# Kernel tuning notes

Hardware: AMD Instinct MI355X
Metric: run time of the kernel (lower is better)

Reference implementation:

```python
import jax, jax.numpy as jnp
import numpy as np

N = 100000      # nodes
E = 1600000     # edges (avg degree 16)
H = 128         # hidden_dim
V = 64          # vector_dim
NUM_LAYERS = 3


def setup_inputs() -> dict:
    key = jax.random.key(0)
    ks = jax.random.split(key, 16)
    s = 0.05
    inp = {
        "node_feats": jax.random.normal(ks[0], (N, 1), dtype=jnp.float32),
        "edge_index": jax.random.randint(ks[1], (2, E), 0, N, dtype=jnp.int64),
        "batch": jnp.zeros((N,), dtype=jnp.int64),
        "temperature": jnp.float32(1.0),
        "t": jnp.float32(1.0),
        # SAGEConv layer 0: in=1 -> out=H. PyG: lin_l (on aggregated, with bias), lin_r (on root, no bias)
        "Wl0": jax.random.normal(ks[2], (1, H), dtype=jnp.float32) * s,
        "bl0": jnp.zeros((H,), dtype=jnp.float32),
        "Wr0": jax.random.normal(ks[3], (1, H), dtype=jnp.float32) * s,
        # SAGEConv layers 1..2: H -> H, stacked
        "Wl": jax.random.normal(ks[4], (NUM_LAYERS - 1, H, H), dtype=jnp.float32) * s,
        "bl": jnp.zeros((NUM_LAYERS - 1, H), dtype=jnp.float32),
        "Wr": jax.random.normal(ks[5], (NUM_LAYERS - 1, H, H), dtype=jnp.float32) * s,
        # to_vector: H -> V
        "Wv": jax.random.normal(ks[6], (H, V), dtype=jnp.float32) * s,
        "bv": jnp.zeros((V,), dtype=jnp.float32),
        # mlp: (V+2) -> H -> 1
        "Wm1": jax.random.normal(ks[7], (V + 2, H), dtype=jnp.float32) * s,
        "bm1": jnp.zeros((H,), dtype=jnp.float32),
        "Wm2": jax.random.normal(ks[8], (H, 1), dtype=jnp.float32) * s,
        "bm2": jnp.zeros((1,), dtype=jnp.float32),
    }
    return inp


def reference(node_feats, edge_index, batch, temperature, t,
              Wl0, bl0, Wr0, Wl, bl, Wr, Wv, bv, Wm1, bm1, Wm2, bm2):
    n = node_feats.shape[0]
    src, dst = edge_index[0], edge_index[1]
    # in-degree for scatter-mean (clamp to 1 for isolated nodes, like PyG mean aggr)
    deg = jax.ops.segment_sum(jnp.ones((src.shape[0],), node_feats.dtype), dst, num_segments=n)
    deg = jnp.maximum(deg, 1.0)[:, None]  # (N,1)

    def sage(h, Wl_, bl_, Wr_):
        # scatter-mean of source features onto destination nodes
        agg = jax.ops.segment_sum(h[src], dst, num_segments=n) / deg
        return agg @ Wl_ + bl_ + h @ Wr_

    h = node_feats.reshape(-1, 1)  # (N,1)
    h = jax.nn.relu(sage(h, Wl0, bl0, Wr0))
    for i in range(Wl.shape[0]):
        h = jax.nn.relu(sage(h, Wl[i], bl[i], Wr[i]))

    # global_mean_pool over single graph (batch all zeros)
    num_graphs = 1
    cnt = jax.ops.segment_sum(jnp.ones((n,), h.dtype), batch, num_segments=num_graphs)
    pooled = jax.ops.segment_sum(h, batch, num_segments=num_graphs) / jnp.maximum(cnt, 1.0)[:, None]  # (1,H)

    z = pooled @ Wv + bv  # (1,V)  (no ReLU in original code path)
    extras = jnp.stack([jnp.asarray(temperature, z.dtype), jnp.asarray(t, z.dtype)]).reshape(1, 2)
    feat = jnp.concatenate([z, extras], axis=1)  # (1, V+2)
    out = jax.nn.softplus(jax.nn.relu(feat @ Wm1 + bm1) @ Wm2 + bm2)  # (1,1)
    return out
```

## Files before the change

kernel.cpp:

```cpp
#include <hip/hip_runtime.h>
#include <hip/hip_bf16.h>
#include <math.h>

#define H 128
#define BKT_SHIFT 9
#define BKT_NODES 512
#define CHUNK 2048
#define GEMM_GRID 512
#define FP8_SCALE 64.0f
#define FP8_INV (1.0f / 64.0f)

typedef __attribute__((ext_vector_type(8))) short short8;
typedef __attribute__((ext_vector_type(4))) float f32x4;
typedef __attribute__((ext_vector_type(2))) float f32x2;

static __device__ __forceinline__ ushort f2b(float v) {
    union { float f; unsigned u; } x; x.f = v;
    unsigned r = x.u + 0x7fffu + ((x.u >> 16) & 1u);
    return (ushort)(r >> 16);
}
static __device__ __forceinline__ float b2f(ushort b) {
    union { unsigned u; float f; } x; x.u = ((unsigned)b) << 16;
    return x.f;
}


__global__ void bucket_hist_kernel(const int* __restrict__ dst, int e,
                                   int* __restrict__ bucketCount, int* __restrict__ blockBase) {
    __shared__ int hist[256];
    int t = threadIdx.x;
    hist[t] = 0;
    __syncthreads();
    int base = blockIdx.x * CHUNK;
    #pragma unroll
    for (int k = 0; k < CHUNK / 256; k++) {
        int i = base + k * 256 + t;
        if (i < e) atomicAdd(&hist[dst[i] >> BKT_SHIFT], 1);
    }
    __syncthreads();
    blockBase[blockIdx.x * 256 + t] = atomicAdd(&bucketCount[t], hist[t]);
}

__global__ void bucket_scan_kernel(const int* __restrict__ bucketCount, int* __restrict__ bucketBase,
                                   int* __restrict__ rs, int n, int e) {
    if (threadIdx.x == 0 && blockIdx.x == 0) {
        int acc = 0;
        for (int i = 0; i < 256; i++) { bucketBase[i] = acc; acc += bucketCount[i]; }
        bucketBase[256] = acc;
        rs[n] = e;
    }
}

__global__ void bucket_scatter_kernel(const int* __restrict__ src, const int* __restrict__ dst, int e,
                                      const int* __restrict__ bucketBase, const int* __restrict__ blockBase,
                                      int2* __restrict__ grouped) {
    __shared__ int cur[256];
    int t = threadIdx.x;
    cur[t] = bucketBase[t] + blockBase[blockIdx.x * 256 + t];
    __syncthreads();
    int base = blockIdx.x * CHUNK;
    #pragma unroll
    for (int k = 0; k < CHUNK / 256; k++) {
        int i = base + k * 256 + t;
        if (i < e) {
            int d = dst[i];
            int pos = atomicAdd(&cur[d >> BKT_SHIFT], 1);
            int2 p; p.x = d; p.y = src[i];
            grouped[pos] = p;
        }
    }
}

__global__ void bucket_csr_kernel(const int2* __restrict__ grouped, const int* __restrict__ bucketBase,
                                  int* __restrict__ rs, int* __restrict__ csr, int n) {
    __shared__ int sdeg[BKT_NODES];
    __shared__ int sexcl[BKT_NODES];
    __shared__ int wsum[4];
    int b = blockIdx.x;
    int t = threadIdx.x;
    int nodeBase = b << BKT_SHIFT;
    int ebase = bucketBase[b], eend = bucketBase[b + 1];
    sdeg[t] = 0; sdeg[t + 256] = 0;
    __syncthreads();
    for (int e = ebase + t; e < eend; e += 256)
        atomicAdd(&sdeg[grouped[e].x - nodeBase], 1);
    __syncthreads();
    int lane = t & 63, wid = t >> 6;
    int v0 = sdeg[2 * t], v1 = sdeg[2 * t + 1];
    int p = v0 + v1;
    int x = p;
    #pragma unroll
    for (int off = 1; off < 64; off <<= 1) {
        int y = __shfl_up(x, off, 64);
        if (lane >= off) x += y;
    }
    if (lane == 63) wsum[wid] = x;
    __syncthreads();
    if (t == 0) {
        int acc = 0;
        #pragma unroll
        for (int w = 0; w < 4; w++) { int tmp = wsum[w]; wsum[w] = acc; acc += tmp; }
    }
    __syncthreads();
    int basep = wsum[wid] + x - p;
    sexcl[2 * t] = basep;
    sexcl[2 * t + 1] = basep + v0;
    int nodes = min(BKT_NODES, n - nodeBase);
    for (int i = t; i < nodes; i += 256) rs[nodeBase + i] = ebase + sexcl[i];
    sdeg[t] = 0; sdeg[t + 256] = 0;
    __syncthreads();
    for (int e = ebase + t; e < eend; e += 256) {
        int2 pr = grouped[e];
        int l = pr.x - nodeBase;
        int r = atomicAdd(&sdeg[l], 1);
        csr[ebase + sexcl[l] + r] = pr.y;
    }
}


__global__ void prep_w_kernel(const float* __restrict__ Wl, const float* __restrict__ Wr,
                              ushort* __restrict__ Btg) {
    int idx = blockIdx.x * 256 + threadIdx.x;
    if (idx >= 65536) return;
    int l = idx >> 15;
    int col = (idx >> 8) & 127;
    int k = idx & 255;
    float v = (k < 128) ? Wl[l * H * H + k * H + col] : Wr[l * H * H + (k - 128) * H + col];
    Btg[idx] = f2b(v);
}


__global__ void agg0_kernel(const float* __restrict__ x, const int* __restrict__ rs,
                            const int* __restrict__ csr, float* __restrict__ agg0, int n) {
    int i = blockIdx.x * 256 + threadIdx.x;
    if (i >= n) return;
    int a = rs[i], b = rs[i + 1];
    float s = 0.f;
    for (int e = a; e < b; e++) s += x[csr[e]];
    agg0[i] = s / (float)max(b - a, 1);
}

__global__ void expand0_kernel(const float* __restrict__ x, const float* __restrict__ agg0,
                               const float* __restrict__ Wl0, const float* __restrict__ bl0,
                               const float* __restrict__ Wr0, ushort* __restrict__ hout,
                               ushort* __restrict__ h8, int n) {
    int idx = blockIdx.x * 256 + threadIdx.x;
    if (idx >= n * 64) return;
    int i = idx >> 6, j = (idx & 63) * 2;
    float gi = agg0[i], xi = x[i];
    float v0 = fmaxf(gi * Wl0[j] + bl0[j] + xi * Wr0[j], 0.f);
    float v1 = fmaxf(gi * Wl0[j + 1] + bl0[j + 1] + xi * Wr0[j + 1], 0.f);
    ushort2 o; o.x = f2b(v0); o.y = f2b(v1);
    *(ushort2*)(hout + (size_t)i * H + j) = o;
    int p = __builtin_amdgcn_cvt_pk_fp8_f32(v0 * FP8_SCALE, v1 * FP8_SCALE, 0, false);
    h8[(size_t)i * 64 + (idx & 63)] = (ushort)p;
}


__global__ void aggregate8_kernel(const unsigned char* __restrict__ h8, const int* __restrict__ rs,
                                  const int* __restrict__ csr, ushort* __restrict__ aggb, int n) {
    int tid = threadIdx.x;
    int w = (tid >> 5) & 1;
    int node = blockIdx.x * 8 + (tid >> 6) * 2 + w;
    if (node >= n) return;
    int sl = (tid >> 3) & 3;
    int fl = tid & 7;
    int a = rs[node], b = rs[node + 1];
    f32x2 s[8];
    #pragma unroll
    for (int j = 0; j < 8; j++) s[j] = (f32x2){0.f, 0.f};

    int e = a;
    for (; e + 8 <= b; e += 8) {
        int n0 = csr[e + sl], n1 = csr[e + 4 + sl];
        uint4 u0 = *(const uint4*)(h8 + (size_t)n0 * 128 + 16 * fl);
        uint4 u1 = *(const uint4*)(h8 + (size_t)n1 * 128 + 16 * fl);
        unsigned dw[8] = {u0.x, u0.y, u0.z, u0.w, u1.x, u1.y, u1.z, u1.w};
        #pragma unroll
        for (int d = 0; d < 8; d++) {
            f32x2 lo = __builtin_amdgcn_cvt_pk_f32_fp8(dw[d], false);
            f32x2 hi = __builtin_amdgcn_cvt_pk_f32_fp8(dw[d], true);
            s[(d & 3) * 2] += lo;
            s[(d & 3) * 2 + 1] += hi;
        }
    }
    for (; e + 4 <= b; e += 4) {
        int n0 = csr[e + sl];
        uint4 u0 = *(const uint4*)(h8 + (size_t)n0 * 128 + 16 * fl);
        unsigned dw[4] = {u0.x, u0.y, u0.z, u0.w};
        #pragma unroll
        for (int d = 0; d < 4; d++) {
            f32x2 lo = __builtin_amdgcn_cvt_pk_f32_fp8(dw[d], false);
            f32x2 hi = __builtin_amdgcn_cvt_pk_f32_fp8(dw[d], true);
            s[d * 2] += lo;
            s[d * 2 + 1] += hi;
        }
    }
    if (e < b && sl < (b - e)) {
        int n0 = csr[e + sl];
        uint4 u0 = *(const uint4*)(h8 + (size_t)n0 * 128 + 16 * fl);
        unsigned dw[4] = {u0.x, u0.y, u0.z, u0.w};
        #pragma unroll
        for (int d = 0; d < 4; d++) {
            f32x2 lo = __builtin_amdgcn_cvt_pk_f32_fp8(dw[d], false);
            f32x2 hi = __builtin_amdgcn_cvt_pk_f32_fp8(dw[d], true);
            s[d * 2] += lo;
            s[d * 2 + 1] += hi;
        }
    }
    #pragma unroll
    for (int j = 0; j < 8; j++) {
        s[j].x += __shfl_xor(s[j].x, 8, 64);
        s[j].y += __shfl_xor(s[j].y, 8, 64);
        s[j].x += __shfl_xor(s[j].x, 16, 64);
        s[j].y += __shfl_xor(s[j].y, 16, 64);
    }
    if (sl == 0) {
        float inv = FP8_INV / (float)max(b - a, 1);
        short8 o0, o1;
        #pragma unroll
        for (int j = 0; j < 4; j++) {
            o0[2 * j]     = (short)f2b(s[j].x * inv);
            o0[2 * j + 1] = (short)f2b(s[j].y * inv);
            o1[2 * j]     = (short)f2b(s[j + 4].x * inv);
            o1[2 * j + 1] = (short)f2b(s[j + 4].y * inv);
        }
        ushort* dstp = aggb + (size_t)node * H + 16 * fl;
        *(short8*)dstp = o0;
        *(short8*)(dstp + 8) = o1;
    }
}


template<bool POOL>
__global__ __launch_bounds__(256, 2) void gemm_kernel(
    const ushort* __restrict__ aggb, const ushort* __restrict__ hb,
    const ushort* __restrict__ Btg,
    const float* __restrict__ bias, ushort* __restrict__ out,
    unsigned char* __restrict__ out8,
    float* __restrict__ partial, int nblk, int n) {
    __shared__ float sums[2][128];
    int tid = threadIdx.x;
    int wave = tid >> 6, lane = tid & 63;
    int l15 = lane & 15, lhi = lane >> 4;
    int colhalf = wave & 1;
    int rowsub = wave >> 1;
    int colbase = colhalf * 64;

    short8 bf[4][8];
    #pragma unroll
    for (int c2 = 0; c2 < 4; c2++) {
        const ushort* wp = Btg + (colbase + c2 * 16 + l15) * 256 + lhi * 8;
        #pragma unroll
        for (int s = 0; s < 8; s++)
            bf[c2][s] = *(const short8*)(wp + s * 32);
    }
    f32x4 bias_v[4];
    #pragma unroll
    for (int c2 = 0; c2 < 4; c2++)
        bias_v[c2] = *(const f32x4*)(bias + colbase + c2 * 16 + lhi * 4);

    f32x4 fs[4];
    #pragma unroll
    for (int c2 = 0; c2 < 4; c2++) fs[c2] = (f32x4){0.f, 0.f, 0.f, 0.f};

    for (int r0 = blockIdx.x * 32; r0 < n; r0 += nblk * 32) {
        int row = r0 + rowsub * 16 + l15;
        int arow = min(row, n - 1);
        short8 af[8];
        #pragma unroll
        for (int s = 0; s < 8; s++)
            af[s] = *(const short8*)((s < 4 ? aggb : hb) + (size_t)arow * H + (s & 3) * 32 + lhi * 8);
        f32x4 acc[4];
        #pragma unroll
        for (int c2 = 0; c2 < 4; c2++) acc[c2] = (f32x4){0.f, 0.f, 0.f, 0.f};
        #pragma unroll
        for (int s = 0; s < 8; s++) {
            #pragma unroll
            for (int c2 = 0; c2 < 4; c2++)
                acc[c2] = __builtin_amdgcn_mfma_f32_16x16x32_bf16(bf[c2][s], af[s], acc[c2], 0, 0, 0);
        }
        if (row < n) {
            if (POOL) {
                #pragma unroll
                for (int c2 = 0; c2 < 4; c2++)
                    #pragma unroll
                    for (int r = 0; r < 4; r++)
                        fs[c2][r] += fmaxf(acc[c2][r] + bias_v[c2][r], 0.f);
            } else {
                #pragma unroll
                for (int c2 = 0; c2 < 4; c2++) {
                    float v0 = fmaxf(acc[c2][0] + bias_v[c2][0], 0.f);
                    float v1 = fmaxf(acc[c2][1] + bias_v[c2][1], 0.f);
                    float v2 = fmaxf(acc[c2][2] + bias_v[c2][2], 0.f);
                    float v3 = fmaxf(acc[c2][3] + bias_v[c2][3], 0.f);
                    ushort4 o;
                    o.x = f2b(v0); o.y = f2b(v1); o.z = f2b(v2); o.w = f2b(v3);
                    *(ushort4*)(out + (size_t)row * H + colbase + c2 * 16 + lhi * 4) = o;
                    int p = __builtin_amdgcn_cvt_pk_fp8_f32(v0 * FP8_SCALE, v1 * FP8_SCALE, 0, false);
                    p = __builtin_amdgcn_cvt_pk_fp8_f32(v2 * FP8_SCALE, v3 * FP8_SCALE, p, true);
                    *(unsigned int*)(out8 + (size_t)row * 128 + colbase + c2 * 16 + lhi * 4) = (unsigned)p;
                }
            }
        }
    }

    if (POOL) {
        #pragma unroll
        for (int c2 = 0; c2 < 4; c2++) {
            #pragma unroll
            for (int m = 1; m < 16; m <<= 1) {
                #pragma unroll
                for (int r = 0; r < 4; r++)
                    fs[c2][r] += __shfl_xor(fs[c2][r], m, 64);
            }
        }
        if (l15 == 0) {
            #pragma unroll
            for (int c2 = 0; c2 < 4; c2++)
                #pragma unroll
                for (int r = 0; r < 4; r++)
                    sums[rowsub][colbase + c2 * 16 + lhi * 4 + r] = fs[c2][r];
        }
        __syncthreads();
        if (tid < 128)
            partial[tid * nblk + blockIdx.x] = sums[0][tid] + sums[1][tid];
    }
}


__global__ void pool_reduce_kernel(const float* __restrict__ partial, float* __restrict__ pooled,
                                   int nb, float invn) {
    int j = blockIdx.x;
    int t = threadIdx.x;
    float s = 0.f;
    for (int b = t; b < nb; b += 64) s += partial[j * nb + b];
    #pragma unroll
    for (int off = 32; off > 0; off >>= 1) s += __shfl_down(s, off, 64);
    if (t == 0) pooled[j] = s * invn;
}


__global__ void mlp_kernel(const float* __restrict__ pooled,
                           const float* __restrict__ Wv, const float* __restrict__ bv,
                           const float* __restrict__ temp, const float* __restrict__ tt,
                           const float* __restrict__ Wm1, const float* __restrict__ bm1,
                           const float* __restrict__ Wm2, const float* __restrict__ bm2,
                           float* __restrict__ out) {
    __shared__ float feat[66];
    __shared__ float red[2];
    int j = threadIdx.x;
    if (j < 64) {
        float s = bv[j];
        for (int k = 0; k < H; k++) s += pooled[k] * Wv[k * 64 + j];
        feat[j] = s;
    }
    if (j == 64) feat[64] = temp[0];
    if (j == 65) feat[65] = tt[0];
    __syncthreads();
    float m = bm1[j];
    for (int k = 0; k < 66; k++) m += feat[k] * Wm1[k * H + j];
    m = fmaxf(m, 0.f);
    float p = m * Wm2[j];
    #pragma unroll
    for (int off = 32; off > 0; off >>= 1) p += __shfl_down(p, off, 64);
    if ((j & 63) == 0) red[j >> 6] = p;
    __syncthreads();
    if (j == 0) {
        float x = red[0] + red[1] + bm2[0];
        out[0] = (x > 20.f) ? x : log1pf(expf(x));
    }
}


extern "C" void kernel_launch(void* const* d_in, const int* in_sizes, int n_in,
                              void* d_out, int out_size, void* d_ws, size_t ws_size,
                              hipStream_t stream) {
    const float* node_feats = (const float*)d_in[0];
    const int* edge_index = (const int*)d_in[1];
    const float* temp = (const float*)d_in[3];
    const float* tt   = (const float*)d_in[4];
    const float* Wl0 = (const float*)d_in[5];
    const float* bl0 = (const float*)d_in[6];
    const float* Wr0 = (const float*)d_in[7];
    const float* Wl  = (const float*)d_in[8];
    const float* bl  = (const float*)d_in[9];
    const float* Wr  = (const float*)d_in[10];
    const float* Wv  = (const float*)d_in[11];
    const float* bv  = (const float*)d_in[12];
    const float* Wm1 = (const float*)d_in[13];
    const float* bm1 = (const float*)d_in[14];
    const float* Wm2 = (const float*)d_in[15];
    const float* bm2 = (const float*)d_in[16];

    const int N = in_sizes[0];
    const int E = in_sizes[1] / 2;
    const int* src = edge_index;
    const int* dst = edge_index + E;

    size_t NH = (size_t)N * H;
    ushort* hA   = (ushort*)d_ws;
    ushort* hB   = hA + NH;
    ushort* aggb = hB + NH;
    ushort* Btg  = aggb + NH;
    float* agg0  = (float*)(Btg + 65536);
    int2* grouped = (int2*)(agg0 + N);
    int* csr     = (int*)(grouped + E);
    int* rs      = csr + E;
    int* bucketCount = rs + (N + 1);
    int* bucketBase  = bucketCount + 256;
    int* blockBase   = bucketBase + 257;
    int NBLK = (E + CHUNK - 1) / CHUNK;
    float* partial = (float*)(blockBase + NBLK * 256);
    float* pooled  = partial + (size_t)H * GEMM_GRID;
    unsigned char* hB8 = (unsigned char*)(pooled + H);
    unsigned char* hA8 = (unsigned char*)grouped;

    int NB = (N + BKT_NODES - 1) / BKT_NODES;

    hipMemsetAsync(bucketCount, 0, 256 * sizeof(int), stream);
    bucket_hist_kernel<<<NBLK, 256, 0, stream>>>(dst, E, bucketCount, blockBase);
    bucket_scan_kernel<<<1, 64, 0, stream>>>(bucketCount, bucketBase, rs, N, E);
    bucket_scatter_kernel<<<NBLK, 256, 0, stream>>>(src, dst, E, bucketBase, blockBase, grouped);
    bucket_csr_kernel<<<NB, 256, 0, stream>>>(grouped, bucketBase, rs, csr, N);

    prep_w_kernel<<<256, 256, 0, stream>>>(Wl, Wr, Btg);

    agg0_kernel<<<(N + 255) / 256, 256, 0, stream>>>(node_feats, rs, csr, agg0, N);
    expand0_kernel<<<((size_t)N * 64 + 255) / 256, 256, 0, stream>>>(
        node_feats, agg0, Wl0, bl0, Wr0, hA, (ushort*)hA8, N);

    aggregate8_kernel<<<(N + 7) / 8, 256, 0, stream>>>(hA8, rs, csr, aggb, N);
    gemm_kernel<false><<<GEMM_GRID, 256, 0, stream>>>(aggb, hA, Btg, bl, hB, hB8, nullptr, GEMM_GRID, N);

    aggregate8_kernel<<<(N + 7) / 8, 256, 0, stream>>>(hB8, rs, csr, aggb, N);
    gemm_kernel<true><<<GEMM_GRID, 256, 0, stream>>>(aggb, hB, Btg + 32768, bl + H, nullptr, nullptr, partial, GEMM_GRID, N);

    pool_reduce_kernel<<<H, 64, 0, stream>>>(partial, pooled, GEMM_GRID, 1.0f / (float)N);
    mlp_kernel<<<1, H, 0, stream>>>(pooled, Wv, bv, temp, tt, Wm1, bm1, Wm2, bm2, (float*)d_out);
}
```

Measured before the change: 259.4 us.

## Store FP8 features and aggregates in 16-byte feature-plane layout per node

Node features (fp8) and aggregated outputs are laid out as 8 planes of 16 features each, so each plane is a compact array of 16-byte rows. Aggregation now uses one thread per node per plane, and blocks are interleaved across planes so each plane's 1.6 MB working set can stay in cache during the random gathers. The GEMM and expand kernels are changed to read and write the planar layout. In exchange, each thread walks the full edge list of its node and repeats the csr index reads once per plane, and the GEMM reads of the aggregate become strided.

```diff
diff --git a/kernel.cpp b/kernel.cpp
--- a/kernel.cpp
+++ b/kernel.cpp
@@ -18,10 +18,6 @@
     union { float f; unsigned u; } x; x.f = v;
     unsigned r = x.u + 0x7fffu + ((x.u >> 16) & 1u);
     return (ushort)(r >> 16);
-}
-static __device__ __forceinline__ float b2f(ushort b) {
-    union { unsigned u; float f; } x; x.u = ((unsigned)b) << 16;
-    return x.f;
 }
 
 
@@ -143,98 +139,92 @@
 __global__ void expand0_kernel(const float* __restrict__ x, const float* __restrict__ agg0,
                                const float* __restrict__ Wl0, const float* __restrict__ bl0,
                                const float* __restrict__ Wr0, ushort* __restrict__ hout,
-                               ushort* __restrict__ h8, int n) {
+                               unsigned char* __restrict__ h8, int n) {
     int idx = blockIdx.x * 256 + threadIdx.x;
-    if (idx >= n * 64) return;
-    int i = idx >> 6, j = (idx & 63) * 2;
+    if (idx >= n * 8) return;
+    int i = idx >> 3, p = idx & 7;
     float gi = agg0[i], xi = x[i];
-    float v0 = fmaxf(gi * Wl0[j] + bl0[j] + xi * Wr0[j], 0.f);
-    float v1 = fmaxf(gi * Wl0[j + 1] + bl0[j + 1] + xi * Wr0[j + 1], 0.f);
-    ushort2 o; o.x = f2b(v0); o.y = f2b(v1);
-    *(ushort2*)(hout + (size_t)i * H + j) = o;
-    int p = __builtin_amdgcn_cvt_pk_fp8_f32(v0 * FP8_SCALE, v1 * FP8_SCALE, 0, false);
-    h8[(size_t)i * 64 + (idx & 63)] = (ushort)p;
-}
-
-
-__global__ void aggregate8_kernel(const unsigned char* __restrict__ h8, const int* __restrict__ rs,
-                                  const int* __restrict__ csr, ushort* __restrict__ aggb, int n) {
-    int tid = threadIdx.x;
-    int w = (tid >> 5) & 1;
-    int node = blockIdx.x * 8 + (tid >> 6) * 2 + w;
+    float v[16];
+    #pragma unroll
+    for (int k = 0; k < 16; k++) {
+        int f = p * 16 + k;
+        v[k] = fmaxf(gi * Wl0[f] + bl0[f] + xi * Wr0[f], 0.f);
+    }
+    short8 o0, o1;
+    #pragma unroll
+    for (int k = 0; k < 8; k++) { o0[k] = (short)f2b(v[k]); o1[k] = (short)f2b(v[k + 8]); }
+    ushort* hp = hout + (size_t)i * H + p * 16;
+    *(short8*)hp = o0;
+    *(short8*)(hp + 8) = o1;
+    uint4 u;
+    unsigned* up = (unsigned*)&u;
+    #pragma unroll
+    for (int d = 0; d < 4; d++) {
+        int pk = __builtin_amdgcn_cvt_pk_fp8_f32(v[4 * d] * FP8_SCALE, v[4 * d + 1] * FP8_SCALE, 0, false);
+        pk = __builtin_amdgcn_cvt_pk_fp8_f32(v[4 * d + 2] * FP8_SCALE, v[4 * d + 3] * FP8_SCALE, pk, true);
+        up[d] = (unsigned)pk;
+    }
+    *(uint4*)(h8 + ((size_t)p * n + i) * 16) = u;
+}
+
+
+__global__ void aggregate_p_kernel(const unsigned char* __restrict__ h8, const int* __restrict__ rs,
+                                   const int* __restrict__ csr, ushort* __restrict__ aggp, int n) {
+    int p = blockIdx.x & 7;
+    int node = (blockIdx.x >> 3) * 256 + threadIdx.x;
     if (node >= n) return;
-    int sl = (tid >> 3) & 3;
-    int fl = tid & 7;
+    const unsigned char* plane = h8 + (size_t)p * n * 16;
     int a = rs[node], b = rs[node + 1];
     f32x2 s[8];
     #pragma unroll
     for (int j = 0; j < 8; j++) s[j] = (f32x2){0.f, 0.f};
-
     int e = a;
-    for (; e + 8 <= b; e += 8) {
-        int n0 = csr[e + sl], n1 = csr[e + 4 + sl];
-        uint4 u0 = *(const uint4*)(h8 + (size_t)n0 * 128 + 16 * fl);
-        uint4 u1 = *(const uint4*)(h8 + (size_t)n1 * 128 + 16 * fl);
-        unsigned dw[8] = {u0.x, u0.y, u0.z, u0.w, u1.x, u1.y, u1.z, u1.w};
-        #pragma unroll
-        for (int d = 0; d < 8; d++) {
-            f32x2 lo = __builtin_amdgcn_cvt_pk_f32_fp8(dw[d], false);
-            f32x2 hi = __builtin_amdgcn_cvt_pk_f32_fp8(dw[d], true);
-            s[(d & 3) * 2] += lo;
-            s[(d & 3) * 2 + 1] += hi;
-        }
-    }
-    for (; e + 4 <= b; e += 4) {
-        int n0 = csr[e + sl];
-        uint4 u0 = *(const uint4*)(h8 + (size_t)n0 * 128 + 16 * fl);
-        unsigned dw[4] = {u0.x, u0.y, u0.z, u0.w};
+    for (; e + 2 <= b; e += 2) {
+        int n0 = csr[e], n1 = csr[e + 1];
+        uint4 u0 = *(const uint4*)(plane + (size_t)n0 * 16);
+        uint4 u1 = *(const uint4*)(plane + (size_t)n1 * 16);
+        unsigned d0[4] = {u0.x, u0.y, u0.z, u0.w};
+        unsigned d1[4] = {u1.x, u1.y, u1.z, u1.w};
         #pragma unroll
         for (int d = 0; d < 4; d++) {
-            f32x2 lo = __builtin_amdgcn_cvt_pk_f32_fp8(dw[d], false);
-            f32x2 hi = __builtin_amdgcn_cvt_pk_f32_fp8(dw[d], true);
-            s[d * 2] += lo;
-            s[d * 2 + 1] += hi;
-        }
-    }
-    if (e < b && sl < (b - e)) {
-        int n0 = csr[e + sl];
-        uint4 u0 = *(const uint4*)(h8 + (size_t)n0 * 128 + 16 * fl);
-        unsigned dw[4] = {u0.x, u0.y, u0.z, u0.w};
+            s[2 * d]     += __builtin_amdgcn_cvt_pk_f32_fp8(d0[d], false);
+            s[2 * d + 1] += __builtin_amdgcn_cvt_pk_f32_fp8(d0[d], true);
+            s[2 * d]     += __builtin_amdgcn_cvt_pk_f32_fp8(d1[d], false);
+            s[2 * d + 1] += __builtin_amdgcn_cvt_pk_f32_fp8(d1[d], true);
+        }
+    }
+    if (e < b) {
+        int n0 = csr[e];
+        uint4 u0 = *(const uint4*)(plane + (size_t)n0 * 16);
+        unsigned d0[4] = {u0.x, u0.y, u0.z, u0.w};
         #pragma unroll
         for (int d = 0; d < 4; d++) {
-            f32x2 lo = __builtin_amdgcn_cvt_pk_f32_fp8(dw[d], false);
-            f32x2 hi = __builtin_amdgcn_cvt_pk_f32_fp8(dw[d], true);
-            s[d * 2] += lo;
-            s[d * 2 + 1] += hi;
-        }
-    }
-    #pragma unroll
-    for (int j = 0; j < 8; j++) {
-        s[j].x += __shfl_xor(s[j].x, 8, 64);
-        s[j].y += __shfl_xor(s[j].y, 8, 64);
-        s[j].x += __shfl_xor(s[j].x, 16, 64);
-        s[j].y += __shfl_xor(s[j].y, 16, 64);
-    }
-    if (sl == 0) {
-        float inv = FP8_INV / (float)max(b - a, 1);
-        short8 o0, o1;
-        #pragma unroll
-        for (int j = 0; j < 4; j++) {
-            o0[2 * j]     = (short)f2b(s[j].x * inv);
-            o0[2 * j + 1] = (short)f2b(s[j].y * inv);
-            o1[2 * j]     = (short)f2b(s[j + 4].x * inv);
-            o1[2 * j + 1] = (short)f2b(s[j + 4].y * inv);
-        }
-        ushort* dstp = aggb + (size_t)node * H + 16 * fl;
-        *(short8*)dstp = o0;
-        *(short8*)(dstp + 8) = o1;
-    }
+            s[2 * d]     += __builtin_amdgcn_cvt_pk_f32_fp8(d0[d], false);
+            s[2 * d + 1] += __builtin_amdgcn_cvt_pk_f32_fp8(d0[d], true);
+        }
+    }
+    float inv = FP8_INV / (float)max(b - a, 1);
+    short8 o0, o1;
+    #pragma unroll
+    for (int d = 0; d < 2; d++) {
+        o0[4 * d]     = (short)f2b(s[2 * d].x * inv);
+        o0[4 * d + 1] = (short)f2b(s[2 * d].y * inv);
+        o0[4 * d + 2] = (short)f2b(s[2 * d + 1].x * inv);
+        o0[4 * d + 3] = (short)f2b(s[2 * d + 1].y * inv);
+        o1[4 * d]     = (short)f2b(s[2 * d + 4].x * inv);
+        o1[4 * d + 1] = (short)f2b(s[2 * d + 4].y * inv);
+        o1[4 * d + 2] = (short)f2b(s[2 * d + 5].x * inv);
+        o1[4 * d + 3] = (short)f2b(s[2 * d + 5].y * inv);
+    }
+    ushort* dstp = aggp + ((size_t)p * n + node) * 16;
+    *(short8*)dstp = o0;
+    *(short8*)(dstp + 8) = o1;
 }
 
 
 template<bool POOL>
 __global__ __launch_bounds__(256, 2) void gemm_kernel(
-    const ushort* __restrict__ aggb, const ushort* __restrict__ hb,
+    const ushort* __restrict__ aggp, const ushort* __restrict__ hb,
     const ushort* __restrict__ Btg,
     const float* __restrict__ bias, ushort* __restrict__ out,
     unsigned char* __restrict__ out8,
@@ -269,8 +259,13 @@
         int arow = min(row, n - 1);
         short8 af[8];
         #pragma unroll
-        for (int s = 0; s < 8; s++)
-            af[s] = *(const short8*)((s < 4 ? aggb : hb) + (size_t)arow * H + (s & 3) * 32 + lhi * 8);
+        for (int s = 0; s < 4; s++) {
+            int f0 = s * 32 + lhi * 8;
+            af[s] = *(const short8*)(aggp + ((size_t)(f0 >> 4) * n + arow) * 16 + (f0 & 15));
+        }
+        #pragma unroll
+        for (int s = 4; s < 8; s++)
+            af[s] = *(const short8*)(hb + (size_t)arow * H + (s & 3) * 32 + lhi * 8);
         f32x4 acc[4];
         #pragma unroll
         for (int c2 = 0; c2 < 4; c2++) acc[c2] = (f32x4){0.f, 0.f, 0.f, 0.f};
@@ -297,9 +292,10 @@
                     ushort4 o;
                     o.x = f2b(v0); o.y = f2b(v1); o.z = f2b(v2); o.w = f2b(v3);
                     *(ushort4*)(out + (size_t)row * H + colbase + c2 * 16 + lhi * 4) = o;
-                    int p = __builtin_amdgcn_cvt_pk_fp8_f32(v0 * FP8_SCALE, v1 * FP8_SCALE, 0, false);
-                    p = __builtin_amdgcn_cvt_pk_fp8_f32(v2 * FP8_SCALE, v3 * FP8_SCALE, p, true);
-                    *(unsigned int*)(out8 + (size_t)row * 128 + colbase + c2 * 16 + lhi * 4) = (unsigned)p;
+                    int pk = __builtin_amdgcn_cvt_pk_fp8_f32(v0 * FP8_SCALE, v1 * FP8_SCALE, 0, false);
+                    pk = __builtin_amdgcn_cvt_pk_fp8_f32(v2 * FP8_SCALE, v3 * FP8_SCALE, pk, true);
+                    int pl = colhalf * 4 + c2;
+                    *(unsigned*)(out8 + ((size_t)pl * n + row) * 16 + lhi * 4) = (unsigned)pk;
                 }
             }
         }
@@ -401,8 +397,8 @@
     size_t NH = (size_t)N * H;
     ushort* hA   = (ushort*)d_ws;
     ushort* hB   = hA + NH;
-    ushort* aggb = hB + NH;
-    ushort* Btg  = aggb + NH;
+    ushort* aggp = hB + NH;
+    ushort* Btg  = aggp + NH;
     float* agg0  = (float*)(Btg + 65536);
     int2* grouped = (int2*)(agg0 + N);
     int* csr     = (int*)(grouped + E);
@@ -427,14 +423,16 @@
     prep_w_kernel<<<256, 256, 0, stream>>>(Wl, Wr, Btg);
 
     agg0_kernel<<<(N + 255) / 256, 256, 0, stream>>>(node_feats, rs, csr, agg0, N);
-    expand0_kernel<<<((size_t)N * 64 + 255) / 256, 256, 0, stream>>>(
-        node_feats, agg0, Wl0, bl0, Wr0, hA, (ushort*)hA8, N);
-
-    aggregate8_kernel<<<(N + 7) / 8, 256, 0, stream>>>(hA8, rs, csr, aggb, N);
-    gemm_kernel<false><<<GEMM_GRID, 256, 0, stream>>>(aggb, hA, Btg, bl, hB, hB8, nullptr, GEMM_GRID, N);
-
-    aggregate8_kernel<<<(N + 7) / 8, 256, 0, stream>>>(hB8, rs, csr, aggb, N);
-    gemm_kernel<true><<<GEMM_GRID, 256, 0, stream>>>(aggb, hB, Btg + 32768, bl + H, nullptr, nullptr, partial, GEMM_GRID, N);
+    expand0_kernel<<<((size_t)N * 8 + 255) / 256, 256, 0, stream>>>(
+        node_feats, agg0, Wl0, bl0, Wr0, hA, hA8, N);
+
+    int AGG_GRID = ((N + 255) / 256) * 8;
+
+    aggregate_p_kernel<<<AGG_GRID, 256, 0, stream>>>(hA8, rs, csr, aggp, N);
+    gemm_kernel<false><<<GEMM_GRID, 256, 0, stream>>>(aggp, hA, Btg, bl, hB, hB8, nullptr, GEMM_GRID, N);
+
+    aggregate_p_kernel<<<AGG_GRID, 256, 0, stream>>>(hB8, rs, csr, aggp, N);
+    gemm_kernel<true><<<GEMM_GRID, 256, 0, stream>>>(aggp, hB, Btg + 32768, bl + H, nullptr, nullptr, partial, GEMM_GRID, N);
 
     pool_reduce_kernel<<<H, 64, 0, stream>>>(partial, pooled, GEMM_GRID, 1.0f / (float)N);
     mlp_kernel<<<1, H, 0, stream>>>(pooled, Wv, bv, temp, tt, Wm1, bm1, Wm2, bm2, (float*)d_out);
```

Result: slower. 332.5 us (+28.2%).
